# Kernel tuning notes

Hardware: AMD Instinct MI355X
Metric: run time of the kernel (lower is better)

The kernel has to match this reference:

```python
import jax, jax.numpy as jnp
import numpy as np
import math

B, T, NQ, NK, D, H = 2, 4, 576, 576, 1024, 16
DH = D // H  # 64 per-head dim
N_POS = (24, 20, 20)          # temporal, y, x rope splits (sum = DH)
CUTOFFS = (256.0, 256.0, 256.0)
CUTOFF_SPATIAL = 0.5
NEG = float(np.finfo(np.float32).min) / 2.0


def _rotate_half(x):
    s = x.shape
    xr = x.reshape(s[:-1] + (s[-1] // 2, 2))
    x1, x2 = xr[..., 0], xr[..., 1]
    return jnp.stack((-x2, x1), axis=-1).reshape(s)


def _co_si(coords, freqs):
    # coords: [B,T,N,3]; freqs[a]: [1,1,n_a/2]
    # NOTE: torch code's scale = 1/sqrt(len(freq)) evaluates to 1.0 since
    # len(param of shape [1,1,n/2]) == 1; we faithfully omit it.
    cos_parts, sin_parts = [], []
    for a, f in enumerate(freqs):
        arg = 0.5 * math.pi * coords[..., a:a + 1] * f[0, 0]  # [B,T,N,n_a/2]
        cos_parts.append(jnp.cos(arg))
        sin_parts.append(jnp.sin(arg))
    return jnp.concatenate(cos_parts, -1), jnp.concatenate(sin_parts, -1)


def _lin(x, W, b):
    # torch nn.Linear: y = x @ W.T + b, W:[out,in]
    return jnp.einsum('...i,oi->...o', x, W) + b


def setup_inputs() -> dict:
    key = jax.random.key(0)
    ks = jax.random.split(key, 16)
    sc = 0.02
    inp = {
        'q_tokens': jax.random.normal(ks[0], (B, T, NQ, D), jnp.float32),
        'kv_tokens': jax.random.normal(ks[1], (B, T, NK, D), jnp.float32),
        'coords_q': jax.random.uniform(ks[2], (B, T, NQ, 3), jnp.float32),
        'coords_k': jax.random.uniform(ks[3], (B, T, NK, 3), jnp.float32),
        'q_pad_mask': jax.random.randint(ks[4], (B, T, NQ), 0, 2).astype(bool),
        'kv_pad_mask': jax.random.randint(ks[5], (B, T, NK), 0, 2).astype(bool),
        'Wq': jax.random.normal(ks[6], (D, D), jnp.float32) * sc,
        'bq': jax.random.normal(ks[7], (D,), jnp.float32) * sc,
        'Wk': jax.random.normal(ks[8], (D, D), jnp.float32) * sc,
        'bk': jax.random.normal(ks[9], (D,), jnp.float32) * sc,
        'Wv': jax.random.normal(ks[10], (D, D), jnp.float32) * sc,
        'bv': jax.random.normal(ks[11], (D,), jnp.float32) * sc,
        'Wo': jax.random.normal(ks[12], (D, D), jnp.float32) * sc,
        'bo': jax.random.normal(ks[13], (D,), jnp.float32) * sc,
        'alpha': jax.random.normal(ks[14], (H,), jnp.float32) * 0.1,
    }
    for i, (c, n) in enumerate(zip(CUTOFFS, N_POS)):
        inp[f'freq{i}'] = jnp.exp(jnp.linspace(0.0, -math.log(c), n // 2)).reshape(1, 1, -1).astype(jnp.float32)
    return inp


def reference(q_tokens, kv_tokens, coords_q, coords_k, q_pad_mask, kv_pad_mask,
              Wq, bq, Wk, bk, Wv, bv, Wo, bo, alpha, freq0, freq1, freq2):
    freqs = (freq0, freq1, freq2)
    # projections -> [B,H,T,N,d]
    q = _lin(q_tokens, Wq, bq).reshape(B, T, NQ, H, DH).transpose(0, 3, 1, 2, 4)
    k = _lin(kv_tokens, Wk, bk).reshape(B, T, NK, H, DH).transpose(0, 3, 1, 2, 4)
    v = _lin(kv_tokens, Wv, bv).reshape(B, T, NK, H, DH).transpose(0, 3, 1, 2, 4)
    # 4D RoPE
    co_q, si_q = _co_si(coords_q, freqs)
    co_k, si_k = _co_si(coords_k, freqs)
    co_q = jnp.repeat(co_q, 2, axis=-1)[:, None]  # [B,1,T,Nq,d]
    si_q = jnp.repeat(si_q, 2, axis=-1)[:, None]
    co_k = jnp.repeat(co_k, 2, axis=-1)[:, None]
    si_k = jnp.repeat(si_k, 2, axis=-1)[:, None]
    q = q * co_q + _rotate_half(q) * si_q
    k = k * co_k + _rotate_half(k) * si_k
    # spatial cdist on (y,x) = last two coord dims -> [B,T,Nq,Nk]
    diff = coords_q[:, :, :, None, 1:] - coords_k[:, :, None, :, 1:]
    dist = jnp.sqrt(jnp.sum(diff * diff, axis=-1))
    bias = jnp.where(dist > CUTOFF_SPATIAL, NEG, 0.0)[:, None]           # cutoff mask
    prior = jnp.exp(-5.0 * dist / CUTOFF_SPATIAL)[:, None]               # v1 distance prior
    bias = bias + alpha[None, :, None, None, None] * prior               # [B,H,T,Nq,Nk]
    ignore = (q_pad_mask[..., :, None] | kv_pad_mask[..., None, :])[:, None]
    bias = jnp.where(ignore, NEG, bias)
    # SDPA per frame
    scores = jnp.einsum('bhtqd,bhtkd->bhtqk', q, k) / math.sqrt(DH) + bias
    attn = jax.nn.softmax(scores, axis=-1)
    y = jnp.einsum('bhtqk,bhtkd->bhtqd', attn, v)
    y = y.transpose(0, 2, 3, 1, 4).reshape(B, T, NQ, D)
    return _lin(y, Wo, bo)
```

## Files before the change

### kernel.cpp

```cpp
#include <hip/hip_runtime.h>
#include <math.h>
#include <stdint.h>

#define BB 2
#define TT 4
#define NQ 576
#define NKV 576
#define DD 1024
#define HH 16
#define DH 64
#define BT (BB*TT)
#define NTOK (BT*NQ)
#define NPAIR ((size_t)BT*NQ*NKV)
#define NEGV (-(3.402823466e38f) * 0.5f)

typedef __attribute__((ext_vector_type(8))) short short8v;
typedef __attribute__((ext_vector_type(4))) float f32x4;

__device__ inline ushort f2bf(float f) {
    union { float f; uint32_t u; } v; v.f = f;
    return (ushort)((v.u + 0x7FFFu + ((v.u >> 16) & 1u)) >> 16);
}

__device__ inline void gld_lds16(const ushort* g, ushort* l) {
    __builtin_amdgcn_global_load_lds(
        (const __attribute__((address_space(1))) unsigned int*)g,
        (__attribute__((address_space(3))) unsigned int*)l, 16, 0, 0);
}

__global__ __launch_bounds__(256) void build_cs_kernel(
    const float* __restrict__ cq, const float* __restrict__ ck,
    const float* __restrict__ f0, const float* __restrict__ f1,
    const float* __restrict__ f2,
    float2* __restrict__ csq, float2* __restrict__ csk)
{
    const int PER = NTOK * 32;
    int idx = blockIdx.x * 256 + threadIdx.x;
    int half = idx / PER;
    int r = idx - half * PER;
    int i = r & 31;
    int tok = r >> 5;
    int axis; float f;
    if (i < 12)      { axis = 0; f = f0[i];      }
    else if (i < 22) { axis = 1; f = f1[i - 12]; }
    else             { axis = 2; f = f2[i - 22]; }
    const float* C = half ? ck : cq;
    float c = C[tok * 3 + axis];
    float arg = __fmul_rn(__fmul_rn(1.57079632679489662f, c), f);
    float s, co;
    __sincosf(arg, &s, &co);
    float2 out; out.x = co; out.y = s;
    (half ? csk : csq)[tok * 32 + i] = out;
}

__global__ __launch_bounds__(576) void prior_kernel(
    const float* __restrict__ cq, const float* __restrict__ ck,
    const uint8_t* __restrict__ qm_raw, const uint8_t* __restrict__ km_raw,
    float* __restrict__ prior, uint8_t* __restrict__ flagb)
{
    __shared__ int flag_s;
    const int tid = threadIdx.x;
    if (tid == 0) flag_s = 0;
    __syncthreads();
    int local = 0;
    for (int j = tid; j < NTOK; j += 576) {
        if ((j & 3) != 0 && (qm_raw[j] | km_raw[j])) local = 1;
    }
    if (local) atomicOr(&flag_s, 1);
    __syncthreads();
    const int is_u8 = flag_s;

    const int bq = blockIdx.x;
    const int kv = tid;
    const int bt = bq / NQ;
    const int kb = bt * NKV + kv;
    uint8_t qmv = is_u8 ? qm_raw[bq] : (uint8_t)(((const int*)qm_raw)[bq] != 0);
    uint8_t kmv = is_u8 ? km_raw[kb] : (uint8_t)(((const int*)km_raw)[kb] != 0);
    const float qy = cq[bq * 3 + 1], qx = cq[bq * 3 + 2];
    const float ky = ck[kb * 3 + 1], kx = ck[kb * 3 + 2];
    float dy = __fsub_rn(qy, ky);
    float dx = __fsub_rn(qx, kx);
    float d2 = __fadd_rn(__fmul_rn(dy, dy), __fmul_rn(dx, dx));
    float dist = __fsqrt_rn(d2);
    int fl = (dist > 0.5f) | qmv | kmv;
    size_t o = (size_t)bq * NKV + kv;
    prior[o] = __expf(-10.f * dist);
    flagb[o] = (uint8_t)fl;
}

#define S4 ((int)((size_t)NTOK * DD / 4))
#define W4 ((int)((size_t)DD * DD / 4))
__global__ __launch_bounds__(256) void f2bf_all_kernel(
    const float* __restrict__ q_tokens, const float* __restrict__ kv_tokens,
    const float* __restrict__ Wq, const float* __restrict__ Wk,
    const float* __restrict__ Wv, const float* __restrict__ Wo,
    ushort* __restrict__ dst0)
{
    int i = blockIdx.x * 256 + threadIdx.x;
    const float* src; int off;
    if (i < 2 * S4) {
        src = (i < S4) ? q_tokens : kv_tokens;
        off = (i < S4) ? i : i - S4;
    } else {
        int j = i - 2 * S4;
        int w = j >> 18;
        src = (w == 0) ? Wq : (w == 1) ? Wk : (w == 2) ? Wv : Wo;
        off = j & (W4 - 1);
    }
    float4 v = ((const float4*)src)[off];
    ushort4 o;
    o.x = f2bf(v.x); o.y = f2bf(v.y); o.z = f2bf(v.z); o.w = f2bf(v.w);
    ((ushort4*)dst0)[i] = o;
}

__device__ __forceinline__ void gemm_core(
    const ushort* __restrict__ X, const ushort* __restrict__ W,
    const float* __restrict__ bias, void* __restrict__ O,
    const float2* __restrict__ cst, const int mode,
    const int m0, const int n0, ushort* As, ushort* Bs)
{
    const int tid = threadIdx.x;
    const int lane = tid & 63, w = tid >> 6;
    const int wm = (w & 1) * 32, wn = (w >> 1) * 64;
    const int frow = lane & 15, quad = lane >> 4;
    const int srow = lane >> 3;
    const int scole = ((lane & 7) ^ srow) << 3;

    f32x4 acc[2][4];
#pragma unroll
    for (int m = 0; m < 2; m++)
#pragma unroll
        for (int n = 0; n < 4; n++) acc[m][n] = (f32x4)0.f;

    for (int k0 = 0; k0 < DD; k0 += 64) {
        __syncthreads();
#pragma unroll
        for (int j = 0; j < 2; j++) {
            int c = w * 2 + j;
            gld_lds16(&X[(size_t)(m0 + c * 8 + srow) * DD + k0 + scole], &As[c * 512]);
        }
#pragma unroll
        for (int j = 0; j < 4; j++) {
            int c = w * 4 + j;
            gld_lds16(&W[(size_t)(n0 + c * 8 + srow) * DD + k0 + scole], &Bs[c * 512]);
        }
        __syncthreads();
        const int rsw = (frow & 7) << 3;
#pragma unroll
        for (int ks = 0; ks < 2; ks++) {
            short8v a[2], b[4];
#pragma unroll
            for (int m = 0; m < 2; m++)
                a[m] = *(const short8v*)&As[(wm + m * 16 + frow) * 64 + ((ks * 32 + quad * 8) ^ rsw)];
#pragma unroll
            for (int n = 0; n < 4; n++)
                b[n] = *(const short8v*)&Bs[(wn + n * 16 + frow) * 64 + ((ks * 32 + quad * 8) ^ rsw)];
#pragma unroll
            for (int m = 0; m < 2; m++)
#pragma unroll
                for (int n = 0; n < 4; n++)
                    acc[m][n] = __builtin_amdgcn_mfma_f32_16x16x32_bf16(
                        a[m], b[n], acc[m][n], 0, 0, 0);
        }
    }

#pragma unroll
    for (int m = 0; m < 2; m++) {
        const int gr0 = m0 + wm + m * 16 + quad * 4;
#pragma unroll
        for (int n = 0; n < 4; n++) {
            const int gc = n0 + wn + n * 16 + frow;
            const float bv_ = bias[gc];
            f32x4 c = acc[m][n];
            if (mode == 1) {
#pragma unroll
                for (int i = 0; i < 4; i++)
                    ((float*)O)[(size_t)(gr0 + i) * DD + gc] = c[i] + bv_;
            } else if (mode == 3) {
                int bt = gr0 / NQ, nn0 = gr0 - bt * NQ;
                int h = gc >> 6, dh = gc & 63;
                ushort4 o4;
                o4.x = f2bf(c[0] + bv_); o4.y = f2bf(c[1] + bv_);
                o4.z = f2bf(c[2] + bv_); o4.w = f2bf(c[3] + bv_);
                *(ushort4*)&((ushort*)O)[(((size_t)(bt * HH + h)) * DH + dh) * NQ + nn0] = o4;
            } else {
                int h = gc >> 6, dh = gc & 63;
                int i2 = dh >> 1;
#pragma unroll
                for (int i = 0; i < 4; i++) {
                    int tok = gr0 + i;
                    float v = c[i] + bv_;
                    float vp = __shfl_xor(v, 1);
                    float2 cs = cst[tok * 32 + i2];
                    float o = (gc & 1) ? (v * cs.x + vp * cs.y)
                                       : (v * cs.x - vp * cs.y);
                    int bt = tok / NQ, nn = tok - bt * NQ;
                    ((ushort*)O)[(((size_t)(bt * HH + h)) * NQ + nn) * DH + dh] = f2bf(o);
                }
            }
        }
    }
}

__global__ __launch_bounds__(256) void gemm_proj3_kernel(
    const ushort* __restrict__ qtb, const ushort* __restrict__ ktb,
    const ushort* __restrict__ Wqb, const ushort* __restrict__ Wkb,
    const ushort* __restrict__ Wvb,
    const float* __restrict__ bq, const float* __restrict__ bk,
    const float* __restrict__ bv,
    ushort* __restrict__ Qh, ushort* __restrict__ Kh, ushort* __restrict__ Vtg,
    const float2* __restrict__ csq, const float2* __restrict__ csk)
{
    __shared__ ushort As[64 * 64];
    __shared__ ushort Bs[128 * 64];
    const int L = blockIdx.x;
    const int xcd = L & 7, j = L >> 3;
    const int mt_g = xcd * 27 + (j >> 3);
    const int nt = j & 7;
    const int seg = mt_g / 72;
    const int smt = mt_g - seg * 72;
    const ushort* X = (seg == 0) ? qtb : ktb;
    const ushort* W = (seg == 0) ? Wqb : (seg == 1) ? Wkb : Wvb;
    const float* bias = (seg == 0) ? bq : (seg == 1) ? bk : bv;
    void* O = (seg == 0) ? (void*)Qh : (seg == 1) ? (void*)Kh : (void*)Vtg;
    const float2* cst = (seg == 0) ? csq : csk;
    const int mode = (seg == 0) ? 4 : (seg == 1) ? 5 : 3;
    gemm_core(X, W, bias, O, cst, mode, smt * 64, nt * 128, As, Bs);
}

__global__ __launch_bounds__(256) void gemm_out_kernel(
    const ushort* __restrict__ Yh, const ushort* __restrict__ Wob,
    const float* __restrict__ bo, float* __restrict__ out)
{
    __shared__ ushort As[64 * 64];
    __shared__ ushort Bs[128 * 64];
    const int L = blockIdx.x;
    const int xcd = L & 7, j = L >> 3;
    const int mt = xcd * 9 + (j >> 3);
    const int nt = j & 7;
    gemm_core(Yh, Wob, bo, (void*)out, nullptr, 1, mt * 64, nt * 128, As, Bs);
}

__global__ __launch_bounds__(256) void attn_mfma_kernel(
    const ushort* __restrict__ Qh, const ushort* __restrict__ Kh,
    const ushort* __restrict__ Vtg,
    const float* __restrict__ prior, const uint8_t* __restrict__ flagb,
    const float* __restrict__ alpha, ushort* __restrict__ Yh)
{
    __shared__ ushort Ks[64][72];
    __shared__ ushort Vt[64][72];
    __shared__ ushort Ps[4][16][88];

    const int tid = threadIdx.x;
    const int lane = tid & 63, w = tid >> 6;
    const int quad = lane >> 4, l15 = lane & 15;

    const int L = blockIdx.x;
    const int xcd = L & 7;
    const int logical = xcd * 144 + (L >> 3);
    const int bh = logical / 9;
    const int qt = logical - bh * 9;
    const int bt = bh >> 4, h = bh & 15;
    const int q0 = qt * 64;

    const size_t hb = ((size_t)(bt * HH + h)) * NQ * DH;
    const size_t vbs = ((size_t)(bt * HH + h)) * DH * NQ;
    const int qg = q0 + w * 16 + l15;

    const ushort* qrow = Qh + hb + (size_t)qg * DH;
    short8v qf0 = *(const short8v*)(qrow + quad * 8);
    short8v qf1 = *(const short8v*)(qrow + 32 + quad * 8);

    const float alph = alpha[h];
    const size_t pbase = ((size_t)(bt * NQ + qg)) * NKV + quad * 4;

    const int krow = tid >> 2, kcol = (tid & 3) * 16;
    const ushort* Ksrc = Kh + hb + (size_t)krow * DH + kcol;
    const ushort* Vsrc = Vtg + vbs + (size_t)krow * NQ + kcol;

    short8v ka0 = *(const short8v*)(Ksrc);
    short8v ka1 = *(const short8v*)(Ksrc + 8);
    short8v va0 = *(const short8v*)(Vsrc);
    short8v va1 = *(const short8v*)(Vsrc + 8);
    float4 prf[4]; uint32_t pfl[4];
#pragma unroll
    for (int jt = 0; jt < 4; jt++) {
        prf[jt] = *(const float4*)&prior[pbase + jt * 16];
        pfl[jt] = *(const uint32_t*)&flagb[pbase + jt * 16];
    }

    float m_run = -INFINITY, l_run = 0.f;
    f32x4 oacc[4];
#pragma unroll
    for (int i = 0; i < 4; i++) oacc[i] = (f32x4)0.f;

    for (int kt = 0; kt < 9; kt++) {
        __syncthreads();
        *(short8v*)&Ks[krow][kcol]     = ka0;
        *(short8v*)&Ks[krow][kcol + 8] = ka1;
        *(short8v*)&Vt[krow][kcol]     = va0;
        *(short8v*)&Vt[krow][kcol + 8] = va1;
        if (kt < 8) {
            const ushort* nk = Ksrc + (size_t)(kt + 1) * 64 * DH;
            const ushort* nv = Vsrc + (size_t)(kt + 1) * 64;
            ka0 = *(const short8v*)(nk);
            ka1 = *(const short8v*)(nk + 8);
            va0 = *(const short8v*)(nv);
            va1 = *(const short8v*)(nv + 8);
        }
        __syncthreads();

        f32x4 sc[4];
#pragma unroll
        for (int jt = 0; jt < 4; jt++) sc[jt] = (f32x4)0.f;
#pragma unroll
        for (int jt = 0; jt < 4; jt++) {
            short8v kf0 = *(const short8v*)&Ks[jt * 16 + l15][quad * 8];
            short8v kf1 = *(const short8v*)&Ks[jt * 16 + l15][32 + quad * 8];
            sc[jt] = __builtin_amdgcn_mfma_f32_16x16x32_bf16(kf0, qf0, sc[jt], 0, 0, 0);
            sc[jt] = __builtin_amdgcn_mfma_f32_16x16x32_bf16(kf1, qf1, sc[jt], 0, 0, 0);
        }

        float p[16];
        float mloc = -INFINITY;
#pragma unroll
        for (int jt = 0; jt < 4; jt++) {
#pragma unroll
            for (int r = 0; r < 4; r++) {
                float prv = (r == 0) ? prf[jt].x : (r == 1) ? prf[jt].y
                          : (r == 2) ? prf[jt].z : prf[jt].w;
                uint8_t fl = (uint8_t)(pfl[jt] >> (8 * r));
                float s = sc[jt][r] * 0.125f + (fl ? NEGV : alph * prv);
                p[jt * 4 + r] = s;
                mloc = fmaxf(mloc, s);
            }
        }
        if (kt < 8) {
            const size_t nb = pbase + (size_t)(kt + 1) * 64;
#pragma unroll
            for (int jt = 0; jt < 4; jt++) {
                prf[jt] = *(const float4*)&prior[nb + jt * 16];
                pfl[jt] = *(const uint32_t*)&flagb[nb + jt * 16];
            }
        }
        mloc = fmaxf(mloc, __shfl_xor(mloc, 16));
        mloc = fmaxf(mloc, __shfl_xor(mloc, 32));
        float m_new = fmaxf(m_run, mloc);
        float scale = __expf(m_run - m_new);
        float psum = 0.f;
#pragma unroll
        for (int i = 0; i < 16; i++) {
            float pv = __expf(p[i] - m_new);
            p[i] = pv;
            psum += pv;
        }
        psum += __shfl_xor(psum, 16);
        psum += __shfl_xor(psum, 32);
        l_run = l_run * scale + psum;
        m_run = m_new;

        float sr[4];
#pragma unroll
        for (int r = 0; r < 4; r++) sr[r] = __shfl(scale, quad * 4 + r);
#pragma unroll
        for (int tdh = 0; tdh < 4; tdh++)
#pragma unroll
            for (int r = 0; r < 4; r++) oacc[tdh][r] *= sr[r];

#pragma unroll
        for (int jt = 0; jt < 4; jt++) {
#pragma unroll
            for (int rp = 0; rp < 2; rp++) {
                uint32_t pk = (uint32_t)f2bf(p[jt * 4 + 2 * rp]) |
                              ((uint32_t)f2bf(p[jt * 4 + 2 * rp + 1]) << 16);
                *(uint32_t*)&Ps[w][l15][jt * 16 + quad * 4 + 2 * rp] = pk;
            }
        }

        short8v pa0 = *(const short8v*)&Ps[w][l15][quad * 8];
        short8v pa1 = *(const short8v*)&Ps[w][l15][32 + quad * 8];
#pragma unroll
        for (int tdh = 0; tdh < 4; tdh++) {
            short8v vb0 = *(const short8v*)&Vt[tdh * 16 + l15][quad * 8];
            short8v vb1 = *(const short8v*)&Vt[tdh * 16 + l15][32 + quad * 8];
            oacc[tdh] = __builtin_amdgcn_mfma_f32_16x16x32_bf16(pa0, vb0, oacc[tdh], 0, 0, 0);
            oacc[tdh] = __builtin_amdgcn_mfma_f32_16x16x32_bf16(pa1, vb1, oacc[tdh], 0, 0, 0);
        }
    }

    float linv = 1.0f / l_run;
    float li[4];
#pragma unroll
    for (int r = 0; r < 4; r++) li[r] = __shfl(linv, quad * 4 + r);
#pragma unroll
    for (int tdh = 0; tdh < 4; tdh++) {
#pragma unroll
        for (int r = 0; r < 4; r++) {
            int tok = bt * NQ + q0 + w * 16 + quad * 4 + r;
            Yh[(size_t)tok * DD + h * DH + tdh * 16 + l15] = f2bf(oacc[tdh][r] * li[r]);
        }
    }
}

extern "C" void kernel_launch(void* const* d_in, const int* in_sizes, int n_in,
                              void* d_out, int out_size, void* d_ws, size_t ws_size,
                              hipStream_t stream)
{
    const float*   q_tokens  = (const float*)d_in[0];
    const float*   kv_tokens = (const float*)d_in[1];
    const float*   coords_q  = (const float*)d_in[2];
    const float*   coords_k  = (const float*)d_in[3];
    const uint8_t* q_pad     = (const uint8_t*)d_in[4];
    const uint8_t* kv_pad    = (const uint8_t*)d_in[5];
    const float*   Wq = (const float*)d_in[6];
    const float*   bq = (const float*)d_in[7];
    const float*   Wk = (const float*)d_in[8];
    const float*   bk = (const float*)d_in[9];
    const float*   Wv = (const float*)d_in[10];
    const float*   bv = (const float*)d_in[11];
    const float*   Wo = (const float*)d_in[12];
    const float*   bo = (const float*)d_in[13];
    const float*   alpha = (const float*)d_in[14];
    const float*   f0 = (const float*)d_in[15];
    const float*   f1 = (const float*)d_in[16];
    const float*   f2 = (const float*)d_in[17];
    float* out = (float*)d_out;

    const size_t SZ = (size_t)NTOK * DD;
    const size_t WSZ = (size_t)DD * DD;
    float2*  csq  = (float2*)d_ws;
    float2*  csk  = csq + (size_t)NTOK * 32;
    float*   prior = (float*)(csk + (size_t)NTOK * 32);
    ushort*  qtb  = (ushort*)(prior + NPAIR);
    ushort*  ktb  = qtb + SZ;
    ushort*  Wqb  = ktb + SZ;
    ushort*  Wkb  = Wqb + WSZ;
    ushort*  Wvb  = Wkb + WSZ;
    ushort*  Wob  = Wvb + WSZ;
    ushort*  Qh   = Wob + WSZ;
    ushort*  Kh   = Qh + SZ;
    ushort*  Vtg  = Kh + SZ;
    ushort*  Yh   = Vtg + SZ;
    uint8_t* flagb = (uint8_t*)(Yh + SZ);

    build_cs_kernel<<<(2 * NTOK * 32) / 256, 256, 0, stream>>>(
        coords_q, coords_k, f0, f1, f2, csq, csk);

    prior_kernel<<<NTOK, 576, 0, stream>>>(
        coords_q, coords_k, q_pad, kv_pad, prior, flagb);

    f2bf_all_kernel<<<(2 * S4 + 4 * W4) / 256, 256, 0, stream>>>(
        q_tokens, kv_tokens, Wq, Wk, Wv, Wo, qtb);

    gemm_proj3_kernel<<<1728, 256, 0, stream>>>(
        qtb, ktb, Wqb, Wkb, Wvb, bq, bk, bv, Qh, Kh, Vtg, csq, csk);

    attn_mfma_kernel<<<1152, 256, 0, stream>>>(
        Qh, Kh, Vtg, prior, flagb, alpha, Yh);

    gemm_out_kernel<<<576, 256, 0, stream>>>(Yh, Wob, bo, out);
}
```

Baseline: 259.1 us.

## Fuse prep kernels, enlarge projection GEMM tile, load K/V directly in attention

Merges the rope table, distance prior/mask and bf16 conversion kernels into one launch that dispatches on block index, removing two kernel launches. The QKV projection GEMM moves from 64x128 to 128x128 tiles (half the blocks, more register accumulators) and drops the XCD-aware block remapping. The attention kernel no longer stages K and V tiles through shared memory with barriers and reads MFMA fragments straight from global memory instead. The risks are uncoalesced or repeated global reads of K/V, lower occupancy from the larger GEMM tile, and poorer L2 locality without the XCD swizzle.

```diff
diff --git a/kernel.cpp b/kernel.cpp
--- a/kernel.cpp
+++ b/kernel.cpp
@@ -28,176 +28,121 @@
         (__attribute__((address_space(3))) unsigned int*)l, 16, 0, 0);
 }
 
-__global__ __launch_bounds__(256) void build_cs_kernel(
-    const float* __restrict__ cq, const float* __restrict__ ck,
-    const float* __restrict__ f0, const float* __restrict__ f1,
-    const float* __restrict__ f2,
-    float2* __restrict__ csq, float2* __restrict__ csk)
-{
-    const int PER = NTOK * 32;
-    int idx = blockIdx.x * 256 + threadIdx.x;
-    int half = idx / PER;
-    int r = idx - half * PER;
-    int i = r & 31;
-    int tok = r >> 5;
-    int axis; float f;
-    if (i < 12)      { axis = 0; f = f0[i];      }
-    else if (i < 22) { axis = 1; f = f1[i - 12]; }
-    else             { axis = 2; f = f2[i - 22]; }
-    const float* C = half ? ck : cq;
-    float c = C[tok * 3 + axis];
-    float arg = __fmul_rn(__fmul_rn(1.57079632679489662f, c), f);
-    float s, co;
-    __sincosf(arg, &s, &co);
-    float2 out; out.x = co; out.y = s;
-    (half ? csk : csq)[tok * 32 + i] = out;
-}
-
-__global__ __launch_bounds__(576) void prior_kernel(
+#define S4 ((int)((size_t)NTOK * DD / 4))
+#define W4 ((int)((size_t)DD * DD / 4))
+#define PRIOR_BLKS NTOK
+#define F2BF_BLKS ((2 * S4 + 4 * W4) / 256)
+#define CS_BLKS ((2 * NTOK * 32) / 256)
+
+__global__ __launch_bounds__(256) void prep_kernel(
     const float* __restrict__ cq, const float* __restrict__ ck,
     const uint8_t* __restrict__ qm_raw, const uint8_t* __restrict__ km_raw,
-    float* __restrict__ prior, uint8_t* __restrict__ flagb)
-{
-    __shared__ int flag_s;
-    const int tid = threadIdx.x;
-    if (tid == 0) flag_s = 0;
-    __syncthreads();
-    int local = 0;
-    for (int j = tid; j < NTOK; j += 576) {
-        if ((j & 3) != 0 && (qm_raw[j] | km_raw[j])) local = 1;
-    }
-    if (local) atomicOr(&flag_s, 1);
-    __syncthreads();
-    const int is_u8 = flag_s;
-
-    const int bq = blockIdx.x;
-    const int kv = tid;
-    const int bt = bq / NQ;
-    const int kb = bt * NKV + kv;
-    uint8_t qmv = is_u8 ? qm_raw[bq] : (uint8_t)(((const int*)qm_raw)[bq] != 0);
-    uint8_t kmv = is_u8 ? km_raw[kb] : (uint8_t)(((const int*)km_raw)[kb] != 0);
-    const float qy = cq[bq * 3 + 1], qx = cq[bq * 3 + 2];
-    const float ky = ck[kb * 3 + 1], kx = ck[kb * 3 + 2];
-    float dy = __fsub_rn(qy, ky);
-    float dx = __fsub_rn(qx, kx);
-    float d2 = __fadd_rn(__fmul_rn(dy, dy), __fmul_rn(dx, dx));
-    float dist = __fsqrt_rn(d2);
-    int fl = (dist > 0.5f) | qmv | kmv;
-    size_t o = (size_t)bq * NKV + kv;
-    prior[o] = __expf(-10.f * dist);
-    flagb[o] = (uint8_t)fl;
-}
-
-#define S4 ((int)((size_t)NTOK * DD / 4))
-#define W4 ((int)((size_t)DD * DD / 4))
-__global__ __launch_bounds__(256) void f2bf_all_kernel(
     const float* __restrict__ q_tokens, const float* __restrict__ kv_tokens,
     const float* __restrict__ Wq, const float* __restrict__ Wk,
     const float* __restrict__ Wv, const float* __restrict__ Wo,
-    ushort* __restrict__ dst0)
-{
-    int i = blockIdx.x * 256 + threadIdx.x;
-    const float* src; int off;
-    if (i < 2 * S4) {
-        src = (i < S4) ? q_tokens : kv_tokens;
-        off = (i < S4) ? i : i - S4;
+    const float* __restrict__ f0, const float* __restrict__ f1,
+    const float* __restrict__ f2,
+    float* __restrict__ prior, uint8_t* __restrict__ flagb,
+    ushort* __restrict__ dst0,
+    float2* __restrict__ csq, float2* __restrict__ csk)
+{
+    const int tid = threadIdx.x;
+    const int B = blockIdx.x;
+    if (B < PRIOR_BLKS) {
+        __shared__ int flag_s;
+        if (tid == 0) flag_s = 0;
+        __syncthreads();
+        int local = 0;
+        for (int j = tid; j < NTOK; j += 256) {
+            if ((j & 3) != 0 && (qm_raw[j] | km_raw[j])) local = 1;
+        }
+        if (local) atomicOr(&flag_s, 1);
+        __syncthreads();
+        const int is_u8 = flag_s;
+        const int bq = B;
+        const int bt = bq / NQ;
+        uint8_t qmv = is_u8 ? qm_raw[bq] : (uint8_t)(((const int*)qm_raw)[bq] != 0);
+        const float qy = cq[bq * 3 + 1], qx = cq[bq * 3 + 2];
+        for (int kv = tid; kv < NKV; kv += 256) {
+            const int kb = bt * NKV + kv;
+            uint8_t kmv = is_u8 ? km_raw[kb] : (uint8_t)(((const int*)km_raw)[kb] != 0);
+            const float ky = ck[kb * 3 + 1], kx = ck[kb * 3 + 2];
+            float dy = __fsub_rn(qy, ky);
+            float dx = __fsub_rn(qx, kx);
+            float d2 = __fadd_rn(__fmul_rn(dy, dy), __fmul_rn(dx, dx));
+            float dist = __fsqrt_rn(d2);
+            int fl = (dist > 0.5f) | qmv | kmv;
+            size_t o = (size_t)bq * NKV + kv;
+            prior[o] = __expf(-10.f * dist);
+            flagb[o] = (uint8_t)fl;
+        }
+    } else if (B < PRIOR_BLKS + F2BF_BLKS) {
+        int i = (B - PRIOR_BLKS) * 256 + tid;
+        const float* src; int off;
+        if (i < 2 * S4) {
+            src = (i < S4) ? q_tokens : kv_tokens;
+            off = (i < S4) ? i : i - S4;
+        } else {
+            int j = i - 2 * S4;
+            int w = j >> 18;
+            src = (w == 0) ? Wq : (w == 1) ? Wk : (w == 2) ? Wv : Wo;
+            off = j & (W4 - 1);
+        }
+        float4 v = ((const float4*)src)[off];
+        ushort4 o;
+        o.x = f2bf(v.x); o.y = f2bf(v.y); o.z = f2bf(v.z); o.w = f2bf(v.w);
+        ((ushort4*)dst0)[i] = o;
     } else {
-        int j = i - 2 * S4;
-        int w = j >> 18;
-        src = (w == 0) ? Wq : (w == 1) ? Wk : (w == 2) ? Wv : Wo;
-        off = j & (W4 - 1);
-    }
-    float4 v = ((const float4*)src)[off];
-    ushort4 o;
-    o.x = f2bf(v.x); o.y = f2bf(v.y); o.z = f2bf(v.z); o.w = f2bf(v.w);
-    ((ushort4*)dst0)[i] = o;
-}
-
-__device__ __forceinline__ void gemm_core(
-    const ushort* __restrict__ X, const ushort* __restrict__ W,
+        const int PER = NTOK * 32;
+        int idx = (B - PRIOR_BLKS - F2BF_BLKS) * 256 + tid;
+        int half = idx / PER;
+        int r = idx - half * PER;
+        int i = r & 31;
+        int tok = r >> 5;
+        int axis; float f;
+        if (i < 12)      { axis = 0; f = f0[i];      }
+        else if (i < 22) { axis = 1; f = f1[i - 12]; }
+        else             { axis = 2; f = f2[i - 22]; }
+        const float* C = half ? ck : cq;
+        float c = C[tok * 3 + axis];
+        float arg = __fmul_rn(__fmul_rn(1.57079632679489662f, c), f);
+        float s, co;
+        __sincosf(arg, &s, &co);
+        float2 out; out.x = co; out.y = s;
+        (half ? csk : csq)[tok * 32 + i] = out;
+    }
+}
+
+__device__ __forceinline__ void gemm_epilogue(
     const float* __restrict__ bias, void* __restrict__ O,
     const float2* __restrict__ cst, const int mode,
-    const int m0, const int n0, ushort* As, ushort* Bs)
-{
-    const int tid = threadIdx.x;
-    const int lane = tid & 63, w = tid >> 6;
-    const int wm = (w & 1) * 32, wn = (w >> 1) * 64;
-    const int frow = lane & 15, quad = lane >> 4;
-    const int srow = lane >> 3;
-    const int scole = ((lane & 7) ^ srow) << 3;
-
-    f32x4 acc[2][4];
-#pragma unroll
-    for (int m = 0; m < 2; m++)
-#pragma unroll
-        for (int n = 0; n < 4; n++) acc[m][n] = (f32x4)0.f;
-
-    for (int k0 = 0; k0 < DD; k0 += 64) {
-        __syncthreads();
-#pragma unroll
-        for (int j = 0; j < 2; j++) {
-            int c = w * 2 + j;
-            gld_lds16(&X[(size_t)(m0 + c * 8 + srow) * DD + k0 + scole], &As[c * 512]);
-        }
-#pragma unroll
-        for (int j = 0; j < 4; j++) {
-            int c = w * 4 + j;
-            gld_lds16(&W[(size_t)(n0 + c * 8 + srow) * DD + k0 + scole], &Bs[c * 512]);
-        }
-        __syncthreads();
-        const int rsw = (frow & 7) << 3;
-#pragma unroll
-        for (int ks = 0; ks < 2; ks++) {
-            short8v a[2], b[4];
-#pragma unroll
-            for (int m = 0; m < 2; m++)
-                a[m] = *(const short8v*)&As[(wm + m * 16 + frow) * 64 + ((ks * 32 + quad * 8) ^ rsw)];
-#pragma unroll
-            for (int n = 0; n < 4; n++)
-                b[n] = *(const short8v*)&Bs[(wn + n * 16 + frow) * 64 + ((ks * 32 + quad * 8) ^ rsw)];
-#pragma unroll
-            for (int m = 0; m < 2; m++)
-#pragma unroll
-                for (int n = 0; n < 4; n++)
-                    acc[m][n] = __builtin_amdgcn_mfma_f32_16x16x32_bf16(
-                        a[m], b[n], acc[m][n], 0, 0, 0);
-        }
-    }
-
-#pragma unroll
-    for (int m = 0; m < 2; m++) {
-        const int gr0 = m0 + wm + m * 16 + quad * 4;
-#pragma unroll
-        for (int n = 0; n < 4; n++) {
-            const int gc = n0 + wn + n * 16 + frow;
-            const float bv_ = bias[gc];
-            f32x4 c = acc[m][n];
-            if (mode == 1) {
-#pragma unroll
-                for (int i = 0; i < 4; i++)
-                    ((float*)O)[(size_t)(gr0 + i) * DD + gc] = c[i] + bv_;
-            } else if (mode == 3) {
-                int bt = gr0 / NQ, nn0 = gr0 - bt * NQ;
-                int h = gc >> 6, dh = gc & 63;
-                ushort4 o4;
-                o4.x = f2bf(c[0] + bv_); o4.y = f2bf(c[1] + bv_);
-                o4.z = f2bf(c[2] + bv_); o4.w = f2bf(c[3] + bv_);
-                *(ushort4*)&((ushort*)O)[(((size_t)(bt * HH + h)) * DH + dh) * NQ + nn0] = o4;
-            } else {
-                int h = gc >> 6, dh = gc & 63;
-                int i2 = dh >> 1;
-#pragma unroll
-                for (int i = 0; i < 4; i++) {
-                    int tok = gr0 + i;
-                    float v = c[i] + bv_;
-                    float vp = __shfl_xor(v, 1);
-                    float2 cs = cst[tok * 32 + i2];
-                    float o = (gc & 1) ? (v * cs.x + vp * cs.y)
-                                       : (v * cs.x - vp * cs.y);
-                    int bt = tok / NQ, nn = tok - bt * NQ;
-                    ((ushort*)O)[(((size_t)(bt * HH + h)) * NQ + nn) * DH + dh] = f2bf(o);
-                }
-            }
+    const int gr0, const int gc, f32x4 c)
+{
+    const float bv_ = bias[gc];
+    if (mode == 1) {
+#pragma unroll
+        for (int i = 0; i < 4; i++)
+            ((float*)O)[(size_t)(gr0 + i) * DD + gc] = c[i] + bv_;
+    } else if (mode == 3) {
+        int bt = gr0 / NQ, nn0 = gr0 - bt * NQ;
+        int h = gc >> 6, dh = gc & 63;
+        ushort4 o4;
+        o4.x = f2bf(c[0] + bv_); o4.y = f2bf(c[1] + bv_);
+        o4.z = f2bf(c[2] + bv_); o4.w = f2bf(c[3] + bv_);
+        *(ushort4*)&((ushort*)O)[(((size_t)(bt * HH + h)) * DH + dh) * NQ + nn0] = o4;
+    } else {
+        int h = gc >> 6, dh = gc & 63;
+        int i2 = dh >> 1;
+#pragma unroll
+        for (int i = 0; i < 4; i++) {
+            int tok = gr0 + i;
+            float v = c[i] + bv_;
+            float vp = __shfl_xor(v, 1);
+            float2 cs = cst[tok * 32 + i2];
+            float o = (gc & 1) ? (v * cs.x + vp * cs.y)
+                               : (v * cs.x - vp * cs.y);
+            int bt = tok / NQ, nn = tok - bt * NQ;
+            ((ushort*)O)[(((size_t)(bt * HH + h)) * NQ + nn) * DH + dh] = f2bf(o);
         }
     }
 }
@@ -211,21 +156,66 @@
     ushort* __restrict__ Qh, ushort* __restrict__ Kh, ushort* __restrict__ Vtg,
     const float2* __restrict__ csq, const float2* __restrict__ csk)
 {
-    __shared__ ushort As[64 * 64];
+    __shared__ ushort As[128 * 64];
     __shared__ ushort Bs[128 * 64];
     const int L = blockIdx.x;
-    const int xcd = L & 7, j = L >> 3;
-    const int mt_g = xcd * 27 + (j >> 3);
-    const int nt = j & 7;
-    const int seg = mt_g / 72;
-    const int smt = mt_g - seg * 72;
+    const int mt_g = L >> 3, nt = L & 7;
+    const int seg = mt_g / 36;
+    const int m0 = (mt_g - seg * 36) * 128, n0 = nt * 128;
     const ushort* X = (seg == 0) ? qtb : ktb;
     const ushort* W = (seg == 0) ? Wqb : (seg == 1) ? Wkb : Wvb;
     const float* bias = (seg == 0) ? bq : (seg == 1) ? bk : bv;
     void* O = (seg == 0) ? (void*)Qh : (seg == 1) ? (void*)Kh : (void*)Vtg;
     const float2* cst = (seg == 0) ? csq : csk;
     const int mode = (seg == 0) ? 4 : (seg == 1) ? 5 : 3;
-    gemm_core(X, W, bias, O, cst, mode, smt * 64, nt * 128, As, Bs);
+
+    const int tid = threadIdx.x;
+    const int lane = tid & 63, w = tid >> 6;
+    const int wm = (w >> 1) * 64, wn = (w & 1) * 64;
+    const int frow = lane & 15, quad = lane >> 4;
+    const int srow = lane >> 3;
+    const int scole = ((lane & 7) ^ srow) << 3;
+
+    f32x4 acc[4][4];
+#pragma unroll
+    for (int m = 0; m < 4; m++)
+#pragma unroll
+        for (int n = 0; n < 4; n++) acc[m][n] = (f32x4)0.f;
+
+    for (int k0 = 0; k0 < DD; k0 += 64) {
+        __syncthreads();
+#pragma unroll
+        for (int j = 0; j < 4; j++) {
+            int c = w * 4 + j;
+            gld_lds16(&X[(size_t)(m0 + c * 8 + srow) * DD + k0 + scole], &As[c * 512]);
+            gld_lds16(&W[(size_t)(n0 + c * 8 + srow) * DD + k0 + scole], &Bs[c * 512]);
+        }
+        __syncthreads();
+        const int rsw = (frow & 7) << 3;
+#pragma unroll
+        for (int ks = 0; ks < 2; ks++) {
+            short8v a[4], b[4];
+#pragma unroll
+            for (int m = 0; m < 4; m++)
+                a[m] = *(const short8v*)&As[(wm + m * 16 + frow) * 64 + ((ks * 32 + quad * 8) ^ rsw)];
+#pragma unroll
+            for (int n = 0; n < 4; n++)
+                b[n] = *(const short8v*)&Bs[(wn + n * 16 + frow) * 64 + ((ks * 32 + quad * 8) ^ rsw)];
+#pragma unroll
+            for (int m = 0; m < 4; m++)
+#pragma unroll
+                for (int n = 0; n < 4; n++)
+                    acc[m][n] = __builtin_amdgcn_mfma_f32_16x16x32_bf16(
+                        a[m], b[n], acc[m][n], 0, 0, 0);
+        }
+    }
+#pragma unroll
+    for (int m = 0; m < 4; m++) {
+        const int gr0 = m0 + wm + m * 16 + quad * 4;
+#pragma unroll
+        for (int n = 0; n < 4; n++)
+            gemm_epilogue(bias, O, cst, mode, gr0, n0 + wn + n * 16 + frow, acc[m][n]);
+    }
 }
 
 __global__ __launch_bounds__(256) void gemm_out_kernel(
@@ -236,9 +226,65 @@
     __shared__ ushort Bs[128 * 64];
     const int L = blockIdx.x;
     const int xcd = L & 7, j = L >> 3;
-    const int mt = xcd * 9 + (j >> 3);
-    const int nt = j & 7;
-    gemm_core(Yh, Wob, bo, (void*)out, nullptr, 1, mt * 64, nt * 128, As, Bs);
+    const int m0 = (xcd * 9 + (j >> 3)) * 64, n0 = (j & 7) * 128;
+
+    const int tid = threadIdx.x;
+    const int lane = tid & 63, w = tid >> 6;
+    const int wm = (w & 1) * 32, wn = (w >> 1) * 64;
+    const int frow = lane & 15, quad = lane >> 4;
+    const int srow = lane >> 3;
+    const int scole = ((lane & 7) ^ srow) << 3;
+
+    f32x4 acc[2][4];
+#pragma unroll
+    for (int m = 0; m < 2; m++)
+#pragma unroll
+        for (int n = 0; n < 4; n++) acc[m][n] = (f32x4)0.f;
+
+    for (int k0 = 0; k0 < DD; k0 += 64) {
+        __syncthreads();
+#pragma unroll
+        for (int j2 = 0; j2 < 2; j2++) {
+            int c = w * 2 + j2;
+            gld_lds16(&Yh[(size_t)(m0 + c * 8 + srow) * DD + k0 + scole], &As[c * 512]);
+        }
+#pragma unroll
+        for (int j2 = 0; j2 < 4; j2++) {
+            int c = w * 4 + j2;
+            gld_lds16(&Wob[(size_t)(n0 + c * 8 + srow) * DD + k0 + scole], &Bs[c * 512]);
+        }
+        __syncthreads();
+        const int rsw = (frow & 7) << 3;
+#pragma unroll
+        for (int ks = 0; ks < 2; ks++) {
+            short8v a[2], b[4];
+#pragma unroll
+            for (int m = 0; m < 2; m++)
+                a[m] = *(const short8v*)&As[(wm + m * 16 + frow) * 64 + ((ks * 32 + quad * 8) ^ rsw)];
+#pragma unroll
+            for (int n = 0; n < 4; n++)
+                b[n] = *(const short8v*)&Bs[(wn + n * 16 + frow) * 64 + ((ks * 32 + quad * 8) ^ rsw)];
+#pragma unroll
+            for (int m = 0; m < 2; m++)
+#pragma unroll
+                for (int n = 0; n < 4; n++)
+                    acc[m][n] = __builtin_amdgcn_mfma_f32_16x16x32_bf16(
+                        a[m], b[n], acc[m][n], 0, 0, 0);
+        }
+    }
+#pragma unroll
+    for (int m = 0; m < 2; m++) {
+        const int gr0 = m0 + wm + m * 16 + quad * 4;
+#pragma unroll
+        for (int n = 0; n < 4; n++) {
+            const int gc = n0 + wn + n * 16 + frow;
+            const float bv_ = bo[gc];
+            f32x4 c = acc[m][n];
+#pragma unroll
+            for (int i = 0; i < 4; i++)
+                out[(size_t)(gr0 + i) * DD + gc] = c[i] + bv_;
+        }
+    }
 }
 
 __global__ __launch_bounds__(256) void attn_mfma_kernel(
@@ -247,8 +293,6 @@
     const float* __restrict__ prior, const uint8_t* __restrict__ flagb,
     const float* __restrict__ alpha, ushort* __restrict__ Yh)
 {
-    __shared__ ushort Ks[64][72];
-    __shared__ ushort Vt[64][72];
     __shared__ ushort Ps[4][16][88];
 
     const int tid = threadIdx.x;
@@ -274,14 +318,6 @@
     const float alph = alpha[h];
     const size_t pbase = ((size_t)(bt * NQ + qg)) * NKV + quad * 4;
 
-    const int krow = tid >> 2, kcol = (tid & 3) * 16;
-    const ushort* Ksrc = Kh + hb + (size_t)krow * DH + kcol;
-    const ushort* Vsrc = Vtg + vbs + (size_t)krow * NQ + kcol;
-
-    short8v ka0 = *(const short8v*)(Ksrc);
-    short8v ka1 = *(const short8v*)(Ksrc + 8);
-    short8v va0 = *(const short8v*)(Vsrc);
-    short8v va1 = *(const short8v*)(Vsrc + 8);
     float4 prf[4]; uint32_t pfl[4];
 #pragma unroll
     for (int jt = 0; jt < 4; jt++) {
@@ -295,28 +331,16 @@
     for (int i = 0; i < 4; i++) oacc[i] = (f32x4)0.f;
 
     for (int kt = 0; kt < 9; kt++) {
-        __syncthreads();
-        *(short8v*)&Ks[krow][kcol]     = ka0;
-        *(short8v*)&Ks[krow][kcol + 8] = ka1;
-        *(short8v*)&Vt[krow][kcol]     = va0;
-        *(short8v*)&Vt[krow][kcol + 8] = va1;
-        if (kt < 8) {
-            const ushort* nk = Ksrc + (size_t)(kt + 1) * 64 * DH;
-            const ushort* nv = Vsrc + (size_t)(kt + 1) * 64;
-            ka0 = *(const short8v*)(nk);
-            ka1 = *(const short8v*)(nk + 8);
-            va0 = *(const short8v*)(nv);
-            va1 = *(const short8v*)(nv + 8);
-        }
-        __syncthreads();
+        const int k0 = kt * 64;
 
         f32x4 sc[4];
 #pragma unroll
         for (int jt = 0; jt < 4; jt++) sc[jt] = (f32x4)0.f;
 #pragma unroll
         for (int jt = 0; jt < 4; jt++) {
-            short8v kf0 = *(const short8v*)&Ks[jt * 16 + l15][quad * 8];
-            short8v kf1 = *(const short8v*)&Ks[jt * 16 + l15][32 + quad * 8];
+            const ushort* krow = Kh + hb + (size_t)(k0 + jt * 16 + l15) * DH;
+            short8v kf0 = *(const short8v*)(krow + quad * 8);
+            short8v kf1 = *(const short8v*)(krow + 32 + quad * 8);
             sc[jt] = __builtin_amdgcn_mfma_f32_16x16x32_bf16(kf0, qf0, sc[jt], 0, 0, 0);
             sc[jt] = __builtin_amdgcn_mfma_f32_16x16x32_bf16(kf1, qf1, sc[jt], 0, 0, 0);
         }
@@ -376,13 +400,14 @@
                 *(uint32_t*)&Ps[w][l15][jt * 16 + quad * 4 + 2 * rp] = pk;
             }
         }
-
         short8v pa0 = *(const short8v*)&Ps[w][l15][quad * 8];
         short8v pa1 = *(const short8v*)&Ps[w][l15][32 + quad * 8];
+
 #pragma unroll
         for (int tdh = 0; tdh < 4; tdh++) {
-            short8v vb0 = *(const short8v*)&Vt[tdh * 16 + l15][quad * 8];
-            short8v vb1 = *(const short8v*)&Vt[tdh * 16 + l15][32 + quad * 8];
+            const ushort* vrow = Vtg + vbs + (size_t)(tdh * 16 + l15) * NQ + k0;
+            short8v vb0 = *(const short8v*)(vrow + quad * 8);
+            short8v vb1 = *(const short8v*)(vrow + 32 + quad * 8);
             oacc[tdh] = __builtin_amdgcn_mfma_f32_16x16x32_bf16(pa0, vb0, oacc[tdh], 0, 0, 0);
             oacc[tdh] = __builtin_amdgcn_mfma_f32_16x16x32_bf16(pa1, vb1, oacc[tdh], 0, 0, 0);
         }
@@ -443,16 +468,12 @@
     ushort*  Yh   = Vtg + SZ;
     uint8_t* flagb = (uint8_t*)(Yh + SZ);
 
-    build_cs_kernel<<<(2 * NTOK * 32) / 256, 256, 0, stream>>>(
-        coords_q, coords_k, f0, f1, f2, csq, csk);
-
-    prior_kernel<<<NTOK, 576, 0, stream>>>(
-        coords_q, coords_k, q_pad, kv_pad, prior, flagb);
-
-    f2bf_all_kernel<<<(2 * S4 + 4 * W4) / 256, 256, 0, stream>>>(
-        q_tokens, kv_tokens, Wq, Wk, Wv, Wo, qtb);
-
-    gemm_proj3_kernel<<<1728, 256, 0, stream>>>(
+    prep_kernel<<<PRIOR_BLKS + F2BF_BLKS + CS_BLKS, 256, 0, stream>>>(
+        coords_q, coords_k, q_pad, kv_pad,
+        q_tokens, kv_tokens, Wq, Wk, Wv, Wo, f0, f1, f2,
+        prior, flagb, qtb, csq, csk);
+
+    gemm_proj3_kernel<<<864, 256, 0, stream>>>(
         qtb, ktb, Wqb, Wkb, Wvb, bq, bk, bv, Qh, Kh, Vtg, csq, csk);
 
     attn_mfma_kernel<<<1152, 256, 0, stream>>>(
```

New measurement: 339.6 us. 1.31x slower.
